# Kernel optimization log

Hardware: AMD Instinct MI355X
Metric: run time of the kernel (lower is better)

## Reference

```python
import jax, jax.numpy as jnp
import numpy as np

S, B, V, E, H, C = 512, 64, 50000, 300, 256, 5


def setup_inputs() -> dict:
    key = jax.random.key(0)
    ks = jax.random.split(key, 8)
    return {
        "inputs": jax.random.randint(ks[0], (S, B), 0, V, dtype=jnp.int64),
        "emb": jax.random.normal(ks[1], (V, E), dtype=jnp.float32),
        # small weight scale to keep tanh out of saturation (matches typical init scale)
        "W_ih": jax.random.normal(ks[2], (H, E), dtype=jnp.float32) * 0.05,
        "W_hh": jax.random.normal(ks[3], (H, H), dtype=jnp.float32) * 0.05,
        "b_ih": jax.random.normal(ks[4], (H,), dtype=jnp.float32) * 0.05,
        "b_hh": jax.random.normal(ks[5], (H,), dtype=jnp.float32) * 0.05,
        "W_out": jax.random.normal(ks[6], (C, H), dtype=jnp.float32) * 0.05,
        "b_out": jax.random.normal(ks[7], (C,), dtype=jnp.float32) * 0.05,
    }


def reference(inputs, emb, W_ih, W_hh, b_ih, b_hh, W_out, b_out):
    # embedding lookup: (S, B, E)
    x = emb[inputs]
    # precompute input-to-hidden projection for all timesteps: (S, B, H)
    xW = jnp.einsum("sbe,he->sbh", x, W_ih) + b_ih

    def step(h, xw_t):
        h_new = jnp.tanh(xw_t + h @ W_hh.T + b_hh)
        return h_new, h_new

    h0 = jnp.zeros((inputs.shape[1], W_hh.shape[0]), dtype=x.dtype)
    _, rnn_out = jax.lax.scan(step, h0, xW)  # (S, B, H)

    logits = jnp.einsum("sbh,ch->sbc", rnn_out, W_out) + b_out  # (S, B, C)
    summed = logits.sum(axis=0)  # (B, C)
    return jax.nn.log_softmax(summed, axis=1)
```

## Files before the change

kernel.cpp:

```cpp
#include <hip/hip_runtime.h>
#include <stdint.h>

#define S_ 512
#define B_ 64
#define V_ 50000
#define E_ 300
#define H_ 256
#define C_ 5

typedef _Float16 h8_t __attribute__((ext_vector_type(8)));
typedef float f32x4 __attribute__((ext_vector_type(4)));

__device__ __forceinline__ float fast_tanh(float x) {
    float e = __builtin_amdgcn_exp2f(x * 2.88539008177793f);
    return fmaf(-2.0f, __builtin_amdgcn_rcpf(e + 1.0f), 1.0f);
}

__device__ __forceinline__ void wait_group(volatile unsigned* gcnt, int grp) {
    while (__hip_atomic_load((const unsigned*)&gcnt[grp], __ATOMIC_RELAXED,
                             __HIP_MEMORY_SCOPE_AGENT) != 64u) {
        __builtin_amdgcn_s_sleep(16);
    }
    __builtin_amdgcn_fence(__ATOMIC_ACQUIRE, "agent");
}

__global__ void wb_prep_kernel(const float* __restrict__ W_ih,
                               uint4* __restrict__ WB) {
    int g = blockIdx.x * 256 + threadIdx.x;
    if (g >= 16 * 10 * 64) return;
    int l = g & 63;
    int ks = (g >> 6) % 10;
    int nt = g / 640;
    int h = nt * 16 + (l & 15);
    int e0 = ks * 32 + (l >> 4) * 8;
    h8_t v;
#pragma unroll
    for (int j = 0; j < 8; ++j) {
        int e = e0 + j;
        v[j] = (e < E_) ? (_Float16)W_ih[(size_t)h * E_ + e] : (_Float16)0.0f;
    }
    WB[g] = __builtin_bit_cast(uint4, v);
}

__global__ __launch_bounds__(512, 2) void fused_kernel(
    const int* __restrict__ idx, const float* __restrict__ emb,
    const uint4* __restrict__ WB, const float* __restrict__ b_ih,
    const float* __restrict__ b_hh, float* __restrict__ xw,
    const float* __restrict__ W_hh, float* __restrict__ hsum_out,
    unsigned* __restrict__ gcnt) {
    __shared__ __attribute__((aligned(16))) unsigned char smem[40960];
    const int tid = threadIdx.x;

    if (blockIdx.x >= 8) {
        const int g = blockIdx.x - 8;
        uint4* Afrag = (uint4*)smem;
        const int w = tid >> 6;
        const int l = tid & 63;
        const int n = l & 15;
        const int hi = l >> 4;
        const int base = g * 64;

        for (int cc = tid; cc < 64 * 40; cc += 512) {
            int m = cc / 40;
            int c = cc - m * 40;
            int ks = c >> 2;
            int hic = c & 3;
            const float* src = emb + (size_t)idx[base + m] * E_ + 8 * c;
            h8_t v;
            if (c < 37) {
                float4 f0 = *(const float4*)src;
                float4 f1 = *(const float4*)(src + 4);
                v[0] = (_Float16)f0.x; v[1] = (_Float16)f0.y;
                v[2] = (_Float16)f0.z; v[3] = (_Float16)f0.w;
                v[4] = (_Float16)f1.x; v[5] = (_Float16)f1.y;
                v[6] = (_Float16)f1.z; v[7] = (_Float16)f1.w;
            } else if (c == 37) {
                float4 f0 = *(const float4*)src;
                v[0] = (_Float16)f0.x; v[1] = (_Float16)f0.y;
                v[2] = (_Float16)f0.z; v[3] = (_Float16)f0.w;
                v[4] = (_Float16)0.0f; v[5] = (_Float16)0.0f;
                v[6] = (_Float16)0.0f; v[7] = (_Float16)0.0f;
            } else {
                v = (h8_t)(_Float16)0.0f;
            }
            int fl = (hic << 4) | (m & 15);
            int mt = m >> 4;
            Afrag[(mt * 10 + ks) * 64 + fl] = __builtin_bit_cast(uint4, v);
        }
        __syncthreads();

        float bias0 = b_ih[w * 32 + n] + b_hh[w * 32 + n];
        float bias1 = b_ih[w * 32 + 16 + n] + b_hh[w * 32 + 16 + n];
        f32x4 c[4][2];
#pragma unroll
        for (int mt = 0; mt < 4; ++mt) {
            c[mt][0] = (f32x4)bias0;
            c[mt][1] = (f32x4)bias1;
        }

        const uint4* wb0 = WB + ((2 * w) * 10) * 64 + l;
        const uint4* wb1 = WB + ((2 * w + 1) * 10) * 64 + l;
#pragma unroll
        for (int ks = 0; ks < 10; ++ks) {
            h8_t b0 = __builtin_bit_cast(h8_t, wb0[ks * 64]);
            h8_t b1 = __builtin_bit_cast(h8_t, wb1[ks * 64]);
#pragma unroll
            for (int mt = 0; mt < 4; ++mt) {
                h8_t a =
                    __builtin_bit_cast(h8_t, Afrag[(mt * 10 + ks) * 64 + l]);
                c[mt][0] = __builtin_amdgcn_mfma_f32_16x16x32_f16(
                    a, b0, c[mt][0], 0, 0, 0);
                c[mt][1] = __builtin_amdgcn_mfma_f32_16x16x32_f16(
                    a, b1, c[mt][1], 0, 0, 0);
            }
        }

#pragma unroll
        for (int mt = 0; mt < 4; ++mt)
#pragma unroll
            for (int q = 0; q < 2; ++q) {
                float* op = xw + (size_t)(base + mt * 16 + hi * 4) * H_ +
                            w * 32 + q * 16 + n;
#pragma unroll
                for (int r = 0; r < 4; ++r) op[(size_t)r * H_] = c[mt][q][r];
            }

        __syncthreads();
        if (tid == 0) {
            __threadfence();
            atomicAdd(&gcnt[g >> 6], 1u);
        }
        return;
    }

    const int w = tid >> 6;
    const int l = tid & 63;
    const int n = l & 15;
    const int hi = l >> 4;
    const int col = n & 7;
    const int sel = n >> 3;
    const int bbase = blockIdx.x * 8;
    const int rowbase = w * 32;

    char* lds = (char*)smem;

    h8_t a[2][8];
#pragma unroll
    for (int mt = 0; mt < 2; ++mt) {
        const float* wr = W_hh + (size_t)(rowbase + mt * 16 + n) * H_;
#pragma unroll
        for (int ks = 0; ks < 8; ++ks) {
            const float* wp = wr + ks * 32 + hi * 8;
            float4 f0 = *(const float4*)wp;
            float4 f1 = *(const float4*)(wp + 4);
            h8_t v;
            v[0] = (_Float16)f0.x; v[1] = (_Float16)f0.y;
            v[2] = (_Float16)f0.z; v[3] = (_Float16)f0.w;
            v[4] = (_Float16)f1.x; v[5] = (_Float16)f1.y;
            v[6] = (_Float16)f1.z; v[7] = (_Float16)f1.w;
            a[mt][ks] = v;
        }
    }

    const int wboff =
        (w * 4 + sel * 2 + (hi >> 1)) * 128 + col * 16 + (hi & 1) * 8;
    const int rdbase = hi * 128 + col * 16;

    for (int t = tid; t < 1024; t += 512) ((unsigned int*)lds)[t] = 0u;

    f32x4 hs = (f32x4)0.0f;

    wait_group(gcnt, 0);

    const float* xwl = xw + (size_t)(bbase + col) * H_ + rowbase + hi * 4;
    f32x4 cv[4][2];
    cv[0][0] = *(const f32x4*)(xwl);
    cv[0][1] = *(const f32x4*)(xwl + 16);
    cv[1][0] = *(const f32x4*)(xwl + 16384);
    cv[1][1] = *(const f32x4*)(xwl + 16384 + 16);
    __syncthreads();

#define STEP(CUR, I, SBASE)                                                    \
    {                                                                          \
        int sp = (SBASE) + 2;                                                  \
        if (sp < S_ && (sp & 63) == 0) wait_group(gcnt, sp >> 6);              \
        if (sp > S_ - 1) sp = S_ - 1;                                          \
        cv[(I + 2) & 3][0] = *(const f32x4*)(xwl + (size_t)sp * 16384);        \
        cv[(I + 2) & 3][1] = *(const f32x4*)(xwl + (size_t)sp * 16384 + 16);   \
        h8_t bf[8];                                                            \
        _Pragma("unroll") for (int ks = 0; ks < 8; ++ks)                       \
            bf[ks] = *(const h8_t*)(lds + (CUR)*4096 + rdbase + ks * 512);     \
        _Pragma("unroll") for (int ks = 0; ks < 8; ++ks) {                     \
            cv[I][0] = __builtin_amdgcn_mfma_f32_16x16x32_f16(                 \
                a[0][ks], bf[ks], cv[I][0], 0, 0, 0);                          \
            cv[I][1] = __builtin_amdgcn_mfma_f32_16x16x32_f16(                 \
                a[1][ks], bf[ks], cv[I][1], 0, 0, 0);                          \
        }                                                                      \
        {                                                                      \
            f32x4 sv = (sel == 0) ? cv[I][0] : cv[I][1];                       \
            float h0 = fast_tanh(sv[0]);                                       \
            float h1 = fast_tanh(sv[1]);                                       \
            float h2 = fast_tanh(sv[2]);                                       \
            float h3 = fast_tanh(sv[3]);                                       \
            hs[0] += h0; hs[1] += h1; hs[2] += h2; hs[3] += h3;                \
            uint2 pk;                                                          \
            pk.x = __builtin_bit_cast(unsigned int,                            \
                                      __builtin_amdgcn_cvt_pkrtz(h0, h1));     \
            pk.y = __builtin_bit_cast(unsigned int,                            \
                                      __builtin_amdgcn_cvt_pkrtz(h2, h3));     \
            *(uint2*)(lds + ((CUR) ^ 1) * 4096 + wboff) = pk;                  \
        }                                                                      \
        asm volatile("s_waitcnt lgkmcnt(0)" ::: "memory");                     \
        __builtin_amdgcn_s_barrier();                                          \
    }

    for (int s = 0; s < S_; s += 4) {
        STEP(0, 0, s)
        STEP(1, 1, s + 1)
        STEP(0, 2, s + 2)
        STEP(1, 3, s + 3)
    }
#undef STEP

    {
        float4 o;
        o.x = hs[0]; o.y = hs[1]; o.z = hs[2]; o.w = hs[3];
        *(float4*)(hsum_out + (size_t)(bbase + col) * H_ + rowbase + sel * 16 +
                   hi * 4) = o;
    }
}

__global__ void out_kernel(const float* __restrict__ hsum,
                           const float* __restrict__ W_out,
                           const float* __restrict__ b_out,
                           float* __restrict__ out) {
    int b = threadIdx.x;
    if (b >= B_) return;
    float logits[C_];
#pragma unroll
    for (int c = 0; c < C_; ++c) {
        float acc = 0.0f;
        for (int k = 0; k < H_; ++k)
            acc = fmaf(hsum[b * H_ + k], W_out[c * H_ + k], acc);
        logits[c] = acc + (float)S_ * b_out[c];
    }
    float m = logits[0];
#pragma unroll
    for (int c = 1; c < C_; ++c) m = fmaxf(m, logits[c]);
    float sum = 0.0f;
#pragma unroll
    for (int c = 0; c < C_; ++c) sum += expf(logits[c] - m);
    float lse = logf(sum);
#pragma unroll
    for (int c = 0; c < C_; ++c) out[b * C_ + c] = logits[c] - m - lse;
}

extern "C" void kernel_launch(void* const* d_in, const int* in_sizes, int n_in,
                              void* d_out, int out_size, void* d_ws,
                              size_t ws_size, hipStream_t stream) {
    const int* idx = (const int*)d_in[0];
    const float* emb = (const float*)d_in[1];
    const float* W_ih = (const float*)d_in[2];
    const float* W_hh = (const float*)d_in[3];
    const float* b_ih = (const float*)d_in[4];
    const float* b_hh = (const float*)d_in[5];
    const float* W_out = (const float*)d_in[6];
    const float* b_out = (const float*)d_in[7];
    float* out = (float*)d_out;

    float* ws = (float*)d_ws;
    uint4* WB = (uint4*)ws;
    float* xw = ws + 40960;
    float* hsum = xw + (size_t)S_ * B_ * H_;
    unsigned* gcnt = (unsigned*)(hsum + B_ * H_);

    hipMemsetAsync(gcnt, 0, 8 * sizeof(unsigned), stream);
    hipLaunchKernelGGL(wb_prep_kernel, dim3(40), dim3(256), 0, stream, W_ih,
                       WB);
    hipLaunchKernelGGL(fused_kernel, dim3(520), dim3(512), 0, stream, idx, emb,
                       WB, b_ih, b_hh, xw, W_hh, hsum, gcnt);
    hipLaunchKernelGGL(out_kernel, dim3(1), dim3(64), 0, stream, hsum, W_out,
                       b_out, out);
}
```

Baseline: 301.1 us.

## Fold weight prep and output head into persistent fused RNN kernel

Removes the separate W_ih fp16 pre-pack kernel and the single-block output kernel. Producer blocks now become persistent: 248 blocks each load their W_ih fragments into registers once and loop over timesteps with stride 248, while the 8 recurrent blocks compute the logits and log-softmax in-kernel using LDS and wave shuffles. This cuts two launches and the WB round-trip through memory, but raises register pressure in the producers and serialises production for some timesteps.

```diff
diff --git a/kernel.cpp b/kernel.cpp
--- a/kernel.cpp
+++ b/kernel.cpp
@@ -7,6 +7,7 @@
 #define E_ 300
 #define H_ 256
 #define C_ 5
+#define NPROD 248
 
 typedef _Float16 h8_t __attribute__((ext_vector_type(8)));
 typedef float f32x4 __attribute__((ext_vector_type(4)));
@@ -16,119 +17,129 @@
     return fmaf(-2.0f, __builtin_amdgcn_rcpf(e + 1.0f), 1.0f);
 }
 
-__device__ __forceinline__ void wait_group(volatile unsigned* gcnt, int grp) {
-    while (__hip_atomic_load((const unsigned*)&gcnt[grp], __ATOMIC_RELAXED,
+__device__ __forceinline__ void wait_group(unsigned* gcnt, int grp) {
+    while (__hip_atomic_load(&gcnt[grp], __ATOMIC_RELAXED,
                              __HIP_MEMORY_SCOPE_AGENT) != 64u) {
         __builtin_amdgcn_s_sleep(16);
     }
     __builtin_amdgcn_fence(__ATOMIC_ACQUIRE, "agent");
 }
 
-__global__ void wb_prep_kernel(const float* __restrict__ W_ih,
-                               uint4* __restrict__ WB) {
-    int g = blockIdx.x * 256 + threadIdx.x;
-    if (g >= 16 * 10 * 64) return;
-    int l = g & 63;
-    int ks = (g >> 6) % 10;
-    int nt = g / 640;
-    int h = nt * 16 + (l & 15);
-    int e0 = ks * 32 + (l >> 4) * 8;
+__device__ __forceinline__ h8_t load_wfrag(const float* __restrict__ W,
+                                           int h, int e0) {
     h8_t v;
-#pragma unroll
-    for (int j = 0; j < 8; ++j) {
-        int e = e0 + j;
-        v[j] = (e < E_) ? (_Float16)W_ih[(size_t)h * E_ + e] : (_Float16)0.0f;
-    }
-    WB[g] = __builtin_bit_cast(uint4, v);
+    if (e0 + 8 <= E_) {
+        float4 f0 = *(const float4*)(W + (size_t)h * E_ + e0);
+        float4 f1 = *(const float4*)(W + (size_t)h * E_ + e0 + 4);
+        v[0] = (_Float16)f0.x; v[1] = (_Float16)f0.y;
+        v[2] = (_Float16)f0.z; v[3] = (_Float16)f0.w;
+        v[4] = (_Float16)f1.x; v[5] = (_Float16)f1.y;
+        v[6] = (_Float16)f1.z; v[7] = (_Float16)f1.w;
+    } else if (e0 < E_) {
+        float4 f0 = *(const float4*)(W + (size_t)h * E_ + e0);
+        v[0] = (_Float16)f0.x; v[1] = (_Float16)f0.y;
+        v[2] = (_Float16)f0.z; v[3] = (_Float16)f0.w;
+        v[4] = (_Float16)0.0f; v[5] = (_Float16)0.0f;
+        v[6] = (_Float16)0.0f; v[7] = (_Float16)0.0f;
+    } else {
+        v = (h8_t)(_Float16)0.0f;
+    }
+    return v;
 }
 
 __global__ __launch_bounds__(512, 2) void fused_kernel(
     const int* __restrict__ idx, const float* __restrict__ emb,
-    const uint4* __restrict__ WB, const float* __restrict__ b_ih,
+    const float* __restrict__ W_ih, const float* __restrict__ b_ih,
     const float* __restrict__ b_hh, float* __restrict__ xw,
-    const float* __restrict__ W_hh, float* __restrict__ hsum_out,
+    const float* __restrict__ W_hh, const float* __restrict__ W_out,
+    const float* __restrict__ b_out, float* __restrict__ out,
     unsigned* __restrict__ gcnt) {
     __shared__ __attribute__((aligned(16))) unsigned char smem[40960];
     const int tid = threadIdx.x;
 
     if (blockIdx.x >= 8) {
-        const int g = blockIdx.x - 8;
+        const int p = blockIdx.x - 8;
         uint4* Afrag = (uint4*)smem;
         const int w = tid >> 6;
         const int l = tid & 63;
         const int n = l & 15;
         const int hi = l >> 4;
-        const int base = g * 64;
-
-        for (int cc = tid; cc < 64 * 40; cc += 512) {
-            int m = cc / 40;
-            int c = cc - m * 40;
-            int ks = c >> 2;
-            int hic = c & 3;
-            const float* src = emb + (size_t)idx[base + m] * E_ + 8 * c;
-            h8_t v;
-            if (c < 37) {
-                float4 f0 = *(const float4*)src;
-                float4 f1 = *(const float4*)(src + 4);
-                v[0] = (_Float16)f0.x; v[1] = (_Float16)f0.y;
-                v[2] = (_Float16)f0.z; v[3] = (_Float16)f0.w;
-                v[4] = (_Float16)f1.x; v[5] = (_Float16)f1.y;
-                v[6] = (_Float16)f1.z; v[7] = (_Float16)f1.w;
-            } else if (c == 37) {
-                float4 f0 = *(const float4*)src;
-                v[0] = (_Float16)f0.x; v[1] = (_Float16)f0.y;
-                v[2] = (_Float16)f0.z; v[3] = (_Float16)f0.w;
-                v[4] = (_Float16)0.0f; v[5] = (_Float16)0.0f;
-                v[6] = (_Float16)0.0f; v[7] = (_Float16)0.0f;
-            } else {
-                v = (h8_t)(_Float16)0.0f;
-            }
-            int fl = (hic << 4) | (m & 15);
-            int mt = m >> 4;
-            Afrag[(mt * 10 + ks) * 64 + fl] = __builtin_bit_cast(uint4, v);
-        }
-        __syncthreads();
-
-        float bias0 = b_ih[w * 32 + n] + b_hh[w * 32 + n];
-        float bias1 = b_ih[w * 32 + 16 + n] + b_hh[w * 32 + 16 + n];
-        f32x4 c[4][2];
-#pragma unroll
-        for (int mt = 0; mt < 4; ++mt) {
-            c[mt][0] = (f32x4)bias0;
-            c[mt][1] = (f32x4)bias1;
-        }
-
-        const uint4* wb0 = WB + ((2 * w) * 10) * 64 + l;
-        const uint4* wb1 = WB + ((2 * w + 1) * 10) * 64 + l;
+
+        h8_t bw0[10], bw1[10];
 #pragma unroll
         for (int ks = 0; ks < 10; ++ks) {
-            h8_t b0 = __builtin_bit_cast(h8_t, wb0[ks * 64]);
-            h8_t b1 = __builtin_bit_cast(h8_t, wb1[ks * 64]);
+            bw0[ks] = load_wfrag(W_ih, (2 * w) * 16 + n, ks * 32 + hi * 8);
+            bw1[ks] = load_wfrag(W_ih, (2 * w + 1) * 16 + n, ks * 32 + hi * 8);
+        }
+        const float bias0 = b_ih[w * 32 + n] + b_hh[w * 32 + n];
+        const float bias1 = b_ih[w * 32 + 16 + n] + b_hh[w * 32 + 16 + n];
+
+        for (int s = p; s < S_; s += NPROD) {
+            const int base = s * 64;
+            __syncthreads();
+            for (int cc = tid; cc < 64 * 40; cc += 512) {
+                int m = cc / 40;
+                int c = cc - m * 40;
+                int ks = c >> 2;
+                int hic = c & 3;
+                const float* src = emb + (size_t)idx[base + m] * E_ + 8 * c;
+                h8_t v;
+                if (c < 37) {
+                    float4 f0 = *(const float4*)src;
+                    float4 f1 = *(const float4*)(src + 4);
+                    v[0] = (_Float16)f0.x; v[1] = (_Float16)f0.y;
+                    v[2] = (_Float16)f0.z; v[3] = (_Float16)f0.w;
+                    v[4] = (_Float16)f1.x; v[5] = (_Float16)f1.y;
+                    v[6] = (_Float16)f1.z; v[7] = (_Float16)f1.w;
+                } else if (c == 37) {
+                    float4 f0 = *(const float4*)src;
+                    v[0] = (_Float16)f0.x; v[1] = (_Float16)f0.y;
+                    v[2] = (_Float16)f0.z; v[3] = (_Float16)f0.w;
+                    v[4] = (_Float16)0.0f; v[5] = (_Float16)0.0f;
+                    v[6] = (_Float16)0.0f; v[7] = (_Float16)0.0f;
+                } else {
+                    v = (h8_t)(_Float16)0.0f;
+                }
+                int fl = (hic << 4) | (m & 15);
+                int mt = m >> 4;
+                Afrag[(mt * 10 + ks) * 64 + fl] = __builtin_bit_cast(uint4, v);
+            }
+            __syncthreads();
+
+            f32x4 c[4][2];
 #pragma unroll
             for (int mt = 0; mt < 4; ++mt) {
-                h8_t a =
-                    __builtin_bit_cast(h8_t, Afrag[(mt * 10 + ks) * 64 + l]);
-                c[mt][0] = __builtin_amdgcn_mfma_f32_16x16x32_f16(
-                    a, b0, c[mt][0], 0, 0, 0);
-                c[mt][1] = __builtin_amdgcn_mfma_f32_16x16x32_f16(
-                    a, b1, c[mt][1], 0, 0, 0);
-            }
-        }
-
-#pragma unroll
-        for (int mt = 0; mt < 4; ++mt)
-#pragma unroll
-            for (int q = 0; q < 2; ++q) {
-                float* op = xw + (size_t)(base + mt * 16 + hi * 4) * H_ +
-                            w * 32 + q * 16 + n;
-#pragma unroll
-                for (int r = 0; r < 4; ++r) op[(size_t)r * H_] = c[mt][q][r];
-            }
-
-        __syncthreads();
-        if (tid == 0) {
-            __threadfence();
-            atomicAdd(&gcnt[g >> 6], 1u);
+                c[mt][0] = (f32x4)bias0;
+                c[mt][1] = (f32x4)bias1;
+            }
+#pragma unroll
+            for (int ks = 0; ks < 10; ++ks) {
+#pragma unroll
+                for (int mt = 0; mt < 4; ++mt) {
+                    h8_t a = __builtin_bit_cast(h8_t,
+                                                Afrag[(mt * 10 + ks) * 64 + l]);
+                    c[mt][0] = __builtin_amdgcn_mfma_f32_16x16x32_f16(
+                        a, bw0[ks], c[mt][0], 0, 0, 0);
+                    c[mt][1] = __builtin_amdgcn_mfma_f32_16x16x32_f16(
+                        a, bw1[ks], c[mt][1], 0, 0, 0);
+                }
+            }
+#pragma unroll
+            for (int mt = 0; mt < 4; ++mt)
+#pragma unroll
+                for (int q = 0; q < 2; ++q) {
+                    float* op = xw + (size_t)(base + mt * 16 + hi * 4) * H_ +
+                                w * 32 + q * 16 + n;
+#pragma unroll
+                    for (int r = 0; r < 4; ++r)
+                        op[(size_t)r * H_] = c[mt][q][r];
+                }
+
+            __syncthreads();
+            if (tid == 0) {
+                __threadfence();
+                atomicAdd(&gcnt[s >> 6], 1u);
+            }
         }
         return;
     }
@@ -223,36 +234,36 @@
 #undef STEP
 
     {
-        float4 o;
-        o.x = hs[0]; o.y = hs[1]; o.z = hs[2]; o.w = hs[3];
-        *(float4*)(hsum_out + (size_t)(bbase + col) * H_ + rowbase + sel * 16 +
-                   hi * 4) = o;
-    }
-}
-
-__global__ void out_kernel(const float* __restrict__ hsum,
-                           const float* __restrict__ W_out,
-                           const float* __restrict__ b_out,
-                           float* __restrict__ out) {
-    int b = threadIdx.x;
-    if (b >= B_) return;
-    float logits[C_];
-#pragma unroll
-    for (int c = 0; c < C_; ++c) {
-        float acc = 0.0f;
-        for (int k = 0; k < H_; ++k)
-            acc = fmaf(hsum[b * H_ + k], W_out[c * H_ + k], acc);
-        logits[c] = acc + (float)S_ * b_out[c];
-    }
-    float m = logits[0];
-#pragma unroll
-    for (int c = 1; c < C_; ++c) m = fmaxf(m, logits[c]);
-    float sum = 0.0f;
-#pragma unroll
-    for (int c = 0; c < C_; ++c) sum += expf(logits[c] - m);
-    float lse = logf(sum);
-#pragma unroll
-    for (int c = 0; c < C_; ++c) out[b * C_ + c] = logits[c] - m - lse;
+        const int k0v = rowbase + sel * 16 + hi * 4;
+        *(f32x4*)(lds + col * 1024 + k0v * 4) = hs;
+    }
+    __syncthreads();
+    {
+        const float* hrow = (const float*)(lds + w * 1024);
+        float lg[C_];
+#pragma unroll
+        for (int c = 0; c < C_; ++c) {
+            float p = 0.0f;
+#pragma unroll
+            for (int q = 0; q < 4; ++q)
+                p = fmaf(hrow[l + 64 * q], W_out[c * H_ + l + 64 * q], p);
+#pragma unroll
+            for (int off = 32; off; off >>= 1) p += __shfl_xor(p, off);
+            lg[c] = p + (float)S_ * b_out[c];
+        }
+        if (l == 0) {
+            float m = lg[0];
+#pragma unroll
+            for (int c = 1; c < C_; ++c) m = fmaxf(m, lg[c]);
+            float sum = 0.0f;
+#pragma unroll
+            for (int c = 0; c < C_; ++c) sum += expf(lg[c] - m);
+            float lse = logf(sum);
+#pragma unroll
+            for (int c = 0; c < C_; ++c)
+                out[(bbase + w) * C_ + c] = lg[c] - m - lse;
+        }
+    }
 }
 
 extern "C" void kernel_launch(void* const* d_in, const int* in_sizes, int n_in,
@@ -269,16 +280,11 @@
     float* out = (float*)d_out;
 
     float* ws = (float*)d_ws;
-    uint4* WB = (uint4*)ws;
-    float* xw = ws + 40960;
-    float* hsum = xw + (size_t)S_ * B_ * H_;
-    unsigned* gcnt = (unsigned*)(hsum + B_ * H_);
+    float* xw = ws;
+    unsigned* gcnt = (unsigned*)(xw + (size_t)S_ * B_ * H_);
 
     hipMemsetAsync(gcnt, 0, 8 * sizeof(unsigned), stream);
-    hipLaunchKernelGGL(wb_prep_kernel, dim3(40), dim3(256), 0, stream, W_ih,
-                       WB);
-    hipLaunchKernelGGL(fused_kernel, dim3(520), dim3(512), 0, stream, idx, emb,
-                       WB, b_ih, b_hh, xw, W_hh, hsum, gcnt);
-    hipLaunchKernelGGL(out_kernel, dim3(1), dim3(64), 0, stream, hsum, W_out,
-                       b_out, out);
-}
+    hipLaunchKernelGGL(fused_kernel, dim3(8 + NPROD), dim3(512), 0, stream,
+                       idx, emb, W_ih, b_ih, b_hh, xw, W_hh, W_out, b_out, out,
+                       gcnt);
+}
```

After: 283.4 us. 1.06x faster.
